# Kernel optimization log

Measured on AMD Instinct MI355X. Metric: run time of the kernel, lower is better.

## Reference

```python
import jax, jax.numpy as jnp
import numpy as np
import math

LOG_2PI = math.log(2.0 * math.pi)

def mv_gaussian_log_prob(value, mu, sig_diags, event_shape):
    # sig_diags acts as per-dim std (matches torch source: diff**2 / sig**2)
    diff = value - mu
    M = jnp.sum((diff / sig_diags) ** 2, axis=-1)
    half_log_det = jnp.sum(jnp.log(sig_diags), axis=-1)
    return -0.5 * (event_shape * LOG_2PI + M) - half_log_det

def setup_inputs() -> dict:
    key = jax.random.key(0)
    ks = jax.random.split(key, 18)
    N, Yd, Xd, K, S = 8192, 512, 64, 16, 10
    d = {}
    d['Y'] = jax.random.normal(ks[0], (N, Yd), jnp.float32)
    d['We_mu'] = jax.random.normal(ks[1], (Yd, Xd), jnp.float32) * 0.05
    d['be_mu'] = jnp.zeros((Xd,), jnp.float32)
    d['We_sig'] = jax.random.normal(ks[2], (Yd, Xd), jnp.float32) * 0.05
    d['be_sig'] = jnp.zeros((Xd,), jnp.float32)
    d['Wd_mu'] = jax.random.normal(ks[3], (Xd, Yd), jnp.float32) * 0.05
    d['bd_mu'] = jnp.zeros((Yd,), jnp.float32)
    d['Wd_sig'] = jax.random.normal(ks[4], (Xd, Yd), jnp.float32) * 0.05
    d['bd_sig'] = jnp.zeros((Yd,), jnp.float32)
    d['phi_mus'] = jax.random.normal(ks[5], (K, Xd), jnp.float32)
    d['phi_sigs'] = jax.random.uniform(ks[6], (K, Xd), jnp.float32, 0.5, 1.5)
    d['phi_logits'] = jax.random.normal(ks[7], (K,), jnp.float32)
    d['theta_mus'] = jax.random.normal(ks[8], (K, Xd), jnp.float32)
    d['theta_sigs'] = jax.random.uniform(ks[9], (K, Xd), jnp.float32, 0.5, 1.5)
    d['theta_logits'] = jax.random.normal(ks[10], (K,), jnp.float32)
    d['u_noise'] = jax.random.uniform(ks[11], (N, S, K), jnp.float32, 1e-6, 1.0 - 1e-6)
    d['eps_noise'] = jax.random.normal(ks[12], (N * S, Xd), jnp.float32)
    d['temperature'] = jnp.ones((1,), jnp.float32)
    return d

def reference(Y, We_mu, be_mu, We_sig, be_sig, Wd_mu, bd_mu, Wd_sig, bd_sig,
              phi_mus, phi_sigs, phi_logits, theta_mus, theta_sigs, theta_logits,
              u_noise, eps_noise, temperature):
    N, Yd = Y.shape
    K, Xd = phi_mus.shape
    S = u_noise.shape[1]
    # encoder: diagonal Gaussian q(x|y)
    enc_mu = Y @ We_mu + be_mu                                   # [N,Xd]
    enc_sig = jax.nn.softplus(Y @ We_sig + be_sig) + 1e-3        # [N,Xd]
    # cluster responsibilities (vectorized over k)
    log_pi = jax.nn.log_softmax(phi_logits)                      # [K]
    std_k = enc_sig[:, None, :] + phi_sigs[None, :, :]           # [N,K,Xd]
    z_logits = log_pi[None, :] + mv_gaussian_log_prob(
        enc_mu[:, None, :], phi_mus[None, :, :], std_k, Xd)      # [N,K]
    z_log_probs = jax.nn.log_softmax(z_logits, axis=-1)
    # per-cluster posterior (diagonal precision-weighted combination)
    inv_enc = 1.0 / enc_sig                                      # [N,Xd]
    inv_gmm = 1.0 / phi_sigs                                     # [K,Xd]
    Sig_t = 1.0 / (inv_enc[:, None, :] + inv_gmm[None, :, :])    # [N,K,Xd]
    mu_t = Sig_t * ((inv_enc * enc_mu)[:, None, :] + (inv_gmm * phi_mus)[None, :, :])
    # relaxed one-hot (gumbel-softmax) samples, probs = exp(z_log_probs)
    g = -jnp.log(-jnp.log(u_noise))                              # [N,S,K]
    z = jax.nn.softmax((z_log_probs[:, None, :] + g) / temperature[0], axis=-1)
    mu_s = jnp.einsum('bsk,bkd->bsd', z, mu_t).reshape(N * S, Xd)
    Sig_s = jnp.einsum('bsk,bkd->bsd', z, Sig_t).reshape(N * S, Xd)
    th_mu = jnp.einsum('bsk,kd->bsd', z, theta_mus).reshape(N * S, Xd)
    th_sig = jnp.einsum('bsk,kd->bsd', z, theta_sigs).reshape(N * S, Xd)
    ph_mu = jnp.einsum('bsk,kd->bsd', z, phi_mus).reshape(N * S, Xd)
    ph_sig = jnp.einsum('bsk,kd->bsd', z, phi_sigs).reshape(N * S, Xd)
    # reparameterized latent samples (diag cov -> std = sqrt)
    x_samp = mu_s + jnp.sqrt(Sig_s) * eps_noise                  # [N*S,Xd]
    # decoder
    mu_y = x_samp @ Wd_mu + bd_mu
    sig_y = jax.nn.softplus(x_samp @ Wd_sig + bd_sig) + 1e-3
    Yr = jnp.broadcast_to(Y[:, None, :], (N, S, Yd)).reshape(N * S, Yd)
    enc_mu_r = jnp.broadcast_to(enc_mu[:, None, :], (N, S, Xd)).reshape(N * S, Xd)
    enc_sig_r = jnp.broadcast_to(enc_sig[:, None, :], (N, S, Xd)).reshape(N * S, Xd)
    zf = z.reshape(N * S, K)
    loss1 = mv_gaussian_log_prob(Yr, mu_y, sig_y, Yd)
    loss2 = -mv_gaussian_log_prob(x_samp, enc_mu_r, enc_sig_r, Xd)
    loss3 = (mv_gaussian_log_prob(x_samp, th_mu, th_sig, Xd)
             + jnp.sum(jax.nn.log_softmax(theta_logits) * zf, axis=1))
    loss4 = -(mv_gaussian_log_prob(x_samp, ph_mu, ph_sig, Xd)
              + jnp.sum((z_log_probs[:, None, :] * z).reshape(N * S, K), axis=1))
    loss5 = jnp.sum(jnp.log(jnp.sum(jnp.exp(z_log_probs), axis=1)))
    return -(jnp.sum(loss1 + loss2 + loss3 + loss4) / S + loss5)
```

## Files before the change

kernel.cpp:

```cpp
#include <hip/hip_runtime.h>
#include <math.h>

#define YD 512
#define XD 64
#define KK 16

typedef __attribute__((ext_vector_type(8))) short short8;
typedef __attribute__((ext_vector_type(4))) float f32x4;

__device__ __forceinline__ float wave_sum(float v) {
#pragma unroll
    for (int off = 32; off > 0; off >>= 1) v += __shfl_xor(v, off, 64);
    return v;
}

__device__ __forceinline__ float fast_rcp(float x) {
    return __builtin_amdgcn_rcpf(x);
}

__device__ __forceinline__ float bcast(float v, int l) {
    return __uint_as_float((unsigned int)__builtin_amdgcn_readlane((int)__float_as_uint(v), l));
}

__device__ __forceinline__ float softplusf(float x) {
    return fmaxf(x, 0.0f) + __logf(1.0f + __expf(-fabsf(x)));
}

__device__ __forceinline__ unsigned short f32_to_bf16(float f) {
    union { float f; unsigned int u; } v; v.f = f;
    unsigned int r = v.u + 0x7fffu + ((v.u >> 16) & 1u);
    return (unsigned short)(r >> 16);
}

__device__ __forceinline__ unsigned int pack2_bf16(float a, float b) {
    unsigned int ua = __float_as_uint(a), ub = __float_as_uint(b);
    ua = (ua + 0x7fffu + ((ua >> 16) & 1u)) >> 16;
    ub = (ub + 0x7fffu + ((ub >> 16) & 1u)) & 0xffff0000u;
    return ua | ub;
}

__global__ __launch_bounds__(256) void prep_kernel(
    const float* __restrict__ Wd_mu, const float* __restrict__ Wd_sig,
    const float* __restrict__ We_mu, const float* __restrict__ We_sig,
    const float* __restrict__ phi_mus, const float* __restrict__ phi_sigs,
    const float* __restrict__ theta_mus, const float* __restrict__ theta_sigs,
    const float* __restrict__ theta_logits,
    unsigned short* __restrict__ wmu_s, unsigned short* __restrict__ wsg_s,
    unsigned short* __restrict__ wenc,
    float4* __restrict__ tab4, float* __restrict__ lsetp)
{
    int idx = blockIdx.x * 256 + threadIdx.x;
    if (idx < 65536) {
        int mat = idx >> 15;
        int e = idx & 32767;
        int j = e & 7;
        int n = (e >> 3) & 15;
        int q = (e >> 7) & 7;
        int tg = e >> 10;
        int k = q * 8 + j;
        int col = tg * 16 + n;
        const float* W = mat ? Wd_sig : Wd_mu;
        unsigned short* o = mat ? wsg_s : wmu_s;
        o[e] = f32_to_bf16(W[k * YD + col]);
    } else if (idx < 131072) {
        int ii = idx - 65536;
        int mat = ii >> 15;
        int e = ii & 32767;
        int j = e & 7;
        int n = (e >> 3) & 15;
        int q = (e >> 7) & 3;
        int ct = (e >> 9) & 3;
        int kt = e >> 11;
        int k = kt * 32 + q * 8 + j;
        int col = ct * 16 + n;
        const float* W = mat ? We_sig : We_mu;
        wenc[mat * 32768 + e] = f32_to_bf16(W[k * XD + col]);
    } else if (idx < 131072 + 1024) {
        int e = idx - 131072;
        float4 t;
        t.x = phi_mus[e];
        t.y = phi_sigs[e];
        t.z = theta_mus[e];
        t.w = theta_sigs[e];
        tab4[e] = t;
    } else if (idx == 131072 + 1024) {
        float mt = theta_logits[0];
        for (int k = 1; k < KK; ++k) mt = fmaxf(mt, theta_logits[k]);
        float st = 0.f;
        for (int k = 0; k < KK; ++k) st += __expf(theta_logits[k] - mt);
        lsetp[0] = mt + __logf(st);
    }
}

__global__ __launch_bounds__(256) void encoder_mfma(
    const float* __restrict__ Y,
    const unsigned short* __restrict__ wenc,
    const float* __restrict__ be_mu, const float* __restrict__ be_sig,
    float* __restrict__ enc_mu, float* __restrict__ enc_sig)
{
    const int t = threadIdx.x;
    const int w = t >> 6, lane = t & 63, l16 = lane & 15, quad = lane >> 4;
    const int mat = blockIdx.x & 1;
    const int rt = blockIdx.x >> 1;
    const int row = rt * 32 + (w >> 1) * 16 + l16;
    const int ct0 = (w & 1) * 2;
    const unsigned short* Ws = wenc + mat * 32768;
    const float4* Yrow = (const float4*)(Y + (size_t)row * YD);

    f32x4 acc0 = (f32x4){0.f, 0.f, 0.f, 0.f};
    f32x4 acc1 = (f32x4){0.f, 0.f, 0.f, 0.f};

#pragma unroll
    for (int kt = 0; kt < 16; ++kt) {
        float4 y0 = Yrow[kt * 8 + quad * 2];
        float4 y1 = Yrow[kt * 8 + quad * 2 + 1];
        union { short8 s; unsigned int u[4]; } a;
        a.u[0] = pack2_bf16(y0.x, y0.y);
        a.u[1] = pack2_bf16(y0.z, y0.w);
        a.u[2] = pack2_bf16(y1.x, y1.y);
        a.u[3] = pack2_bf16(y1.z, y1.w);
        short8 b0 = *(const short8*)(Ws + (((kt * 4 + ct0) * 4 + quad) * 16 + l16) * 8);
        short8 b1 = *(const short8*)(Ws + (((kt * 4 + ct0 + 1) * 4 + quad) * 16 + l16) * 8);
        acc0 = __builtin_amdgcn_mfma_f32_16x16x32_bf16(a.s, b0, acc0, 0, 0, 0);
        acc1 = __builtin_amdgcn_mfma_f32_16x16x32_bf16(a.s, b1, acc1, 0, 0, 0);
    }

    const float* bias = mat ? be_sig : be_mu;
    float* outp = mat ? enc_sig : enc_mu;
    const int base_row = rt * 32 + (w >> 1) * 16 + quad * 4;
#pragma unroll
    for (int h = 0; h < 2; ++h) {
        int col = (ct0 + h) * 16 + l16;
        float bv = bias[col];
        f32x4 acc = h ? acc1 : acc0;
#pragma unroll
        for (int r = 0; r < 4; ++r) {
            float v = acc[r] + bv;
            if (mat) v = softplusf(v) + 1e-3f;
            outp[(size_t)(base_row + r) * XD + col] = v;
        }
    }
}

__global__ __launch_bounds__(256) void resp_kernel(
    const float* __restrict__ enc_mu_g, const float* __restrict__ enc_sig_g,
    const float* __restrict__ phi_mus, const float* __restrict__ phi_sigs,
    const float* __restrict__ phi_logits,
    float* __restrict__ zlp, double* __restrict__ slotsL5)
{
    __shared__ float red[4];
    const int wv = threadIdx.x >> 6;
    const int n = blockIdx.x * 4 + wv;
    const int lane = threadIdx.x & 63;
    const int kk = lane & 15;
    const int g = lane >> 4;

    const float4* em4 = (const float4*)(enc_mu_g + (size_t)n * XD + g * 16);
    const float4* es4 = (const float4*)(enc_sig_g + (size_t)n * XD + g * 16);
    const float4* pm4 = (const float4*)(phi_mus + kk * XD + g * 16);
    const float4* ps4 = (const float4*)(phi_sigs + kk * XD + g * 16);

    float part = 0.f;
#pragma unroll
    for (int q = 0; q < 4; ++q) {
        float4 em = em4[q], es = es4[q], pm = pm4[q], ps = ps4[q];
        {
            float sd = es.x + ps.x; float df = (em.x - pm.x) * fast_rcp(sd);
            part += fmaf(-0.5f * df, df, -__logf(sd));
        }
        {
            float sd = es.y + ps.y; float df = (em.y - pm.y) * fast_rcp(sd);
            part += fmaf(-0.5f * df, df, -__logf(sd));
        }
        {
            float sd = es.z + ps.z; float df = (em.z - pm.z) * fast_rcp(sd);
            part += fmaf(-0.5f * df, df, -__logf(sd));
        }
        {
            float sd = es.w + ps.w; float df = (em.w - pm.w) * fast_rcp(sd);
            part += fmaf(-0.5f * df, df, -__logf(sd));
        }
    }
    part += __shfl_xor(part, 16, 64);
    part += __shfl_xor(part, 32, 64);
    float zl = part + phi_logits[kk];

    float m = zl;
#pragma unroll
    for (int off = 1; off <= 8; off <<= 1) m = fmaxf(m, __shfl_xor(m, off, 64));
    float e = __expf(zl - m);
    float s = e;
#pragma unroll
    for (int off = 1; off <= 8; off <<= 1) s += __shfl_xor(s, off, 64);
    zl -= m + __logf(s);

    float m3 = zl;
#pragma unroll
    for (int off = 1; off <= 8; off <<= 1) m3 = fmaxf(m3, __shfl_xor(m3, off, 64));
    float e3 = __expf(zl - m3);
    float s3 = e3;
#pragma unroll
    for (int off = 1; off <= 8; off <<= 1) s3 += __shfl_xor(s3, off, 64);
    float l5 = m3 + __logf(s3);

    if (lane < KK) zlp[(size_t)n * KK + lane] = zl;

    if (lane == 0) red[wv] = l5;
    __syncthreads();
    if (threadIdx.x == 0) {
        float tt = red[0] + red[1] + red[2] + red[3];
        atomicAdd(slotsL5 + (blockIdx.x & 63), (double)tt);
    }
}

__global__ __launch_bounds__(256, 6) void sample_kernel(
    const float* __restrict__ enc_mu_g, const float* __restrict__ enc_sig_g,
    const float* __restrict__ zlp, const float4* __restrict__ tab4,
    const float* __restrict__ theta_logits, const float* __restrict__ lsetp,
    const float* __restrict__ u_noise, const float* __restrict__ eps_noise,
    const float* __restrict__ temperature,
    unsigned short* __restrict__ x_bf16, double* __restrict__ slots234,
    unsigned int magicS)
{
    __shared__ float red[4];
    const int wv = threadIdx.x >> 6;
    const int wid = blockIdx.x * 4 + wv;
    const int d = threadIdx.x & 63;
    const int n = (int)(((unsigned long long)(unsigned int)wid * magicS) >> 35);

    const int kd = d & 15;
    const float invT = fast_rcp(temperature[0]);
    float zlk = zlp[(size_t)n * KK + kd];
    float u   = u_noise[(size_t)wid * KK + kd];
    float tlk = theta_logits[kd];
    float lgk = (zlk - __logf(-__logf(u))) * invT;
    float mg = lgk;
    mg = fmaxf(mg, __shfl_xor(mg, 1, 64));
    mg = fmaxf(mg, __shfl_xor(mg, 2, 64));
    mg = fmaxf(mg, __shfl_xor(mg, 4, 64));
    mg = fmaxf(mg, __shfl_xor(mg, 8, 64));
    float ek = __expf(lgk - mg);
    float zs = ek;
    float pz = ek * zlk;
    float pt = ek * tlk;
#pragma unroll
    for (int off = 1; off <= 8; off <<= 1) {
        zs += __shfl_xor(zs, off, 64);
        pz += __shfl_xor(pz, off, 64);
        pt += __shfl_xor(pt, off, 64);
    }
    const float rn   = fast_rcp(bcast(zs, 0));
    const float dzS  = bcast(pz, 0) * rn;
    const float dthS = bcast(pt, 0) * rn;

    const float em = enc_mu_g[(size_t)n * XD + d];
    const float es = enc_sig_g[(size_t)n * XD + d];
    const float inv_es = fast_rcp(es);
    const float log_es = __logf(es);
    const float em_ie = inv_es * em;

    float ms = 0.f, Ss = 0.f, tmu = 0.f, tsig = 0.f, pmu = 0.f, psig = 0.f;
#pragma unroll
    for (int k = 0; k < KK; ++k) {
        float e_k = bcast(ek, k);
        float4 tb = tab4[k * XD + d];
        float ig = fast_rcp(tb.y);
        float Sg = fast_rcp(inv_es + ig);
        float mu = Sg * fmaf(ig, tb.x, em_ie);
        ms   = fmaf(e_k, mu, ms);
        Ss   = fmaf(e_k, Sg, Ss);
        tmu  = fmaf(e_k, tb.z, tmu);
        tsig = fmaf(e_k, tb.w, tsig);
        pmu  = fmaf(e_k, tb.x, pmu);
        psig = fmaf(e_k, tb.y, psig);
    }
    ms *= rn; Ss *= rn; tmu *= rn; tsig *= rn; pmu *= rn; psig *= rn;

    float ep = eps_noise[(size_t)wid * XD + d];
    float x = fmaf(__builtin_amdgcn_sqrtf(Ss), ep, ms);
    x_bf16[(size_t)wid * XD + d] = f32_to_bf16(x);

    float de  = (x - em) * inv_es;
    float dt2 = (x - tmu) * fast_rcp(tsig);
    float dp  = (x - pmu) * fast_rcp(psig);
    float r = 0.5f * (de * de - dt2 * dt2 + dp * dp)
            + log_es - __logf(tsig) + __logf(psig);
    r = wave_sum(r);

    const float C234 = 0.5f * XD * 1.8378770664093453f;
    float acc = r + C234 + (dthS - lsetp[0]) - dzS;

    if (d == 0) red[wv] = acc;
    __syncthreads();
    if (threadIdx.x == 0) {
        float t = red[0] + red[1] + red[2] + red[3];
        atomicAdd(slots234 + (blockIdx.x & 63), (double)t);
    }
}

__global__ __launch_bounds__(256) void decoder_mfma(
    const unsigned short* __restrict__ xb,
    const unsigned short* __restrict__ wmu_s,
    const unsigned short* __restrict__ wsg_s,
    const float* __restrict__ bd_mu, const float* __restrict__ bd_sig,
    const float* __restrict__ Y, double* __restrict__ slots1,
    unsigned int magicS)
{
    __shared__ float red[4];
    const int t = threadIdx.x;
    const int w = t >> 6;
    const int lane = t & 63;
    const int l16 = lane & 15;
    const int quad = lane >> 4;
    const int mb = blockIdx.x >> 3;
    const int nb = blockIdx.x & 7;

    const int mrow = mb * 64 + w * 16 + l16;
    const short8 a0 = *(const short8*)(xb + (size_t)mrow * XD + quad * 8);
    const short8 a1 = *(const short8*)(xb + (size_t)mrow * XD + 32 + quad * 8);

    f32x4 accmu[4], accsg[4];
#pragma unroll
    for (int tt = 0; tt < 4; ++tt) {
        accmu[tt] = (f32x4){0.f, 0.f, 0.f, 0.f};
        accsg[tt] = (f32x4){0.f, 0.f, 0.f, 0.f};
    }

#pragma unroll
    for (int tt = 0; tt < 4; ++tt) {
        int tg = nb * 4 + tt;
        int boff = ((tg * 8 + quad) * 16 + l16) * 8;
        short8 b0 = *(const short8*)(wmu_s + boff);
        short8 b1 = *(const short8*)(wmu_s + boff + 512);
        short8 c0 = *(const short8*)(wsg_s + boff);
        short8 c1 = *(const short8*)(wsg_s + boff + 512);
        accmu[tt] = __builtin_amdgcn_mfma_f32_16x16x32_bf16(a0, b0, accmu[tt], 0, 0, 0);
        accmu[tt] = __builtin_amdgcn_mfma_f32_16x16x32_bf16(a1, b1, accmu[tt], 0, 0, 0);
        accsg[tt] = __builtin_amdgcn_mfma_f32_16x16x32_bf16(a0, c0, accsg[tt], 0, 0, 0);
        accsg[tt] = __builtin_amdgcn_mfma_f32_16x16x32_bf16(a1, c1, accsg[tt], 0, 0, 0);
    }

    float part = 0.f;
    const int m_base = mb * 64 + w * 16 + quad * 4;
#pragma unroll
    for (int tt = 0; tt < 4; ++tt) {
        int col = (nb * 4 + tt) * 16 + l16;
        float bmv = bd_mu[col], bsv = bd_sig[col];
#pragma unroll
        for (int r = 0; r < 4; ++r) {
            int row = m_base + r;
            unsigned int ny = (unsigned int)(((unsigned long long)(unsigned int)row * magicS) >> 35);
            float Yv = Y[(size_t)ny * YD + col];
            float sig = softplusf(accsg[tt][r] + bsv) + 1e-3f;
            float diff = (Yv - (accmu[tt][r] + bmv)) * fast_rcp(sig);
            part = fmaf(-0.5f * diff, diff, part) - __logf(sig);
        }
    }
    part = wave_sum(part);
    if (lane == 0) red[w] = part;
    __syncthreads();
    if (t == 0) {
        atomicAdd(slots1 + (blockIdx.x & 63),
                  (double)(red[0] + red[1] + red[2] + red[3]));
    }
}

__global__ void finalize_kernel(const double* __restrict__ slots,
                                float* __restrict__ out, int NS, int S)
{
    double l234 = 0.0, l5 = 0.0, l1 = 0.0;
    for (int i = 0; i < 64; ++i) {
        l234 += slots[i];
        l5   += slots[64 + i];
        l1   += slots[128 + i];
    }
    l1 += (double)NS * (-0.5 * (double)YD * 1.8378770664093453);
    out[0] = (float)(-((l1 + l234) / (double)S + l5));
}

extern "C" void kernel_launch(void* const* d_in, const int* in_sizes, int n_in,
                              void* d_out, int out_size, void* d_ws, size_t ws_size,
                              hipStream_t stream) {
    const float* Y            = (const float*)d_in[0];
    const float* We_mu        = (const float*)d_in[1];
    const float* be_mu        = (const float*)d_in[2];
    const float* We_sig       = (const float*)d_in[3];
    const float* be_sig       = (const float*)d_in[4];
    const float* Wd_mu        = (const float*)d_in[5];
    const float* bd_mu        = (const float*)d_in[6];
    const float* Wd_sig       = (const float*)d_in[7];
    const float* bd_sig       = (const float*)d_in[8];
    const float* phi_mus      = (const float*)d_in[9];
    const float* phi_sigs     = (const float*)d_in[10];
    const float* phi_logits   = (const float*)d_in[11];
    const float* theta_mus    = (const float*)d_in[12];
    const float* theta_sigs   = (const float*)d_in[13];
    const float* theta_logits = (const float*)d_in[14];
    const float* u_noise      = (const float*)d_in[15];
    const float* eps_noise    = (const float*)d_in[16];
    const float* temperature  = (const float*)d_in[17];

    const int N = in_sizes[0] / YD;
    const int S = in_sizes[15] / (N * KK);
    const int NS = N * S;
    const unsigned int magicS =
        (unsigned int)((((unsigned long long)1 << 35) + S - 1) / (unsigned long long)S);

    char* base = (char*)d_ws;
    double* slots = (double*)base;
    float* enc_mu  = (float*)(base + 2048);
    float* enc_sig = enc_mu + (size_t)N * XD;
    float* zlp     = enc_sig + (size_t)N * XD;
    float4* tab4   = (float4*)(zlp + (size_t)N * KK);
    float* lsetp   = (float*)(tab4 + 1024);
    unsigned short* xb    = (unsigned short*)(lsetp + 16);
    unsigned short* wmu_s = xb + (size_t)NS * XD;
    unsigned short* wsg_s = wmu_s + 32768;
    unsigned short* wenc  = wsg_s + 32768;

    hipMemsetAsync(slots, 0, 2048, stream);

    prep_kernel<<<517, 256, 0, stream>>>(Wd_mu, Wd_sig, We_mu, We_sig,
                                         phi_mus, phi_sigs, theta_mus,
                                         theta_sigs, theta_logits,
                                         wmu_s, wsg_s, wenc, tab4, lsetp);
    encoder_mfma<<<(N / 32) * 2, 256, 0, stream>>>(Y, wenc, be_mu, be_sig,
                                                   enc_mu, enc_sig);
    resp_kernel<<<N / 4, 256, 0, stream>>>(enc_mu, enc_sig, phi_mus, phi_sigs,
                                           phi_logits, zlp, slots + 64);
    sample_kernel<<<NS / 4, 256, 0, stream>>>(enc_mu, enc_sig, zlp, tab4,
                                              theta_logits, lsetp,
                                              u_noise, eps_noise, temperature,
                                              xb, slots, magicS);
    decoder_mfma<<<(NS / 64) * (YD / 64), 256, 0, stream>>>(
        xb, wmu_s, wsg_s, bd_mu, bd_sig, Y, slots + 128, magicS);
    finalize_kernel<<<1, 1, 0, stream>>>(slots, (float*)d_out, NS, S);
}
```

Before: 240.3 us.

## Process all samples per data row in sample kernel, reusing per-cluster posterior terms

The sample kernel now assigns one wave per data row and loops over all S samples, so the per-cluster posterior mean/variance, theta/phi tables and encoder stats are computed and loaded once per row instead of once per sample. Gumbel-softmax weights for up to four samples are computed in parallel across 16-lane groups. Register use rises (six 16-entry arrays), so the occupancy hint drops from 6 to 3. The encoder is split into one 16-column tile per wave with twice as many blocks, and biases are folded into the MFMA accumulator init in both the encoder and decoder.

```diff
diff --git a/kernel.cpp b/kernel.cpp
--- a/kernel.cpp
+++ b/kernel.cpp
@@ -4,6 +4,7 @@
 #define YD 512
 #define XD 64
 #define KK 16
+#define SS 10
 
 typedef __attribute__((ext_vector_type(8))) short short8;
 typedef __attribute__((ext_vector_type(4))) float f32x4;
@@ -102,13 +103,16 @@
     const int w = t >> 6, lane = t & 63, l16 = lane & 15, quad = lane >> 4;
     const int mat = blockIdx.x & 1;
     const int rt = blockIdx.x >> 1;
-    const int row = rt * 32 + (w >> 1) * 16 + l16;
-    const int ct0 = (w & 1) * 2;
+    const int row = rt * 16 + l16;
+    const int ct = w;
     const unsigned short* Ws = wenc + mat * 32768;
     const float4* Yrow = (const float4*)(Y + (size_t)row * YD);
 
-    f32x4 acc0 = (f32x4){0.f, 0.f, 0.f, 0.f};
-    f32x4 acc1 = (f32x4){0.f, 0.f, 0.f, 0.f};
+    const float* bias = mat ? be_sig : be_mu;
+    float* outp = mat ? enc_sig : enc_mu;
+    const int col = ct * 16 + l16;
+    const float bv = bias[col];
+    f32x4 acc = (f32x4){bv, bv, bv, bv};
 
 #pragma unroll
     for (int kt = 0; kt < 16; ++kt) {
@@ -119,26 +123,16 @@
         a.u[1] = pack2_bf16(y0.z, y0.w);
         a.u[2] = pack2_bf16(y1.x, y1.y);
         a.u[3] = pack2_bf16(y1.z, y1.w);
-        short8 b0 = *(const short8*)(Ws + (((kt * 4 + ct0) * 4 + quad) * 16 + l16) * 8);
-        short8 b1 = *(const short8*)(Ws + (((kt * 4 + ct0 + 1) * 4 + quad) * 16 + l16) * 8);
-        acc0 = __builtin_amdgcn_mfma_f32_16x16x32_bf16(a.s, b0, acc0, 0, 0, 0);
-        acc1 = __builtin_amdgcn_mfma_f32_16x16x32_bf16(a.s, b1, acc1, 0, 0, 0);
-    }
-
-    const float* bias = mat ? be_sig : be_mu;
-    float* outp = mat ? enc_sig : enc_mu;
-    const int base_row = rt * 32 + (w >> 1) * 16 + quad * 4;
-#pragma unroll
-    for (int h = 0; h < 2; ++h) {
-        int col = (ct0 + h) * 16 + l16;
-        float bv = bias[col];
-        f32x4 acc = h ? acc1 : acc0;
-#pragma unroll
-        for (int r = 0; r < 4; ++r) {
-            float v = acc[r] + bv;
-            if (mat) v = softplusf(v) + 1e-3f;
-            outp[(size_t)(base_row + r) * XD + col] = v;
-        }
+        short8 b = *(const short8*)(Ws + (((kt * 4 + ct) * 4 + quad) * 16 + l16) * 8);
+        acc = __builtin_amdgcn_mfma_f32_16x16x32_bf16(a.s, b, acc, 0, 0, 0);
+    }
+
+    const int base_row = rt * 16 + quad * 4;
+#pragma unroll
+    for (int r = 0; r < 4; ++r) {
+        float v = acc[r];
+        if (mat) v = softplusf(v) + 1e-3f;
+        outp[(size_t)(base_row + r) * XD + col] = v;
     }
 }
 
@@ -213,45 +207,24 @@
     }
 }
 
-__global__ __launch_bounds__(256, 6) void sample_kernel(
+__global__ __launch_bounds__(256, 3) void sample_kernel(
     const float* __restrict__ enc_mu_g, const float* __restrict__ enc_sig_g,
     const float* __restrict__ zlp, const float4* __restrict__ tab4,
     const float* __restrict__ theta_logits, const float* __restrict__ lsetp,
     const float* __restrict__ u_noise, const float* __restrict__ eps_noise,
     const float* __restrict__ temperature,
-    unsigned short* __restrict__ x_bf16, double* __restrict__ slots234,
-    unsigned int magicS)
+    unsigned short* __restrict__ x_bf16, double* __restrict__ slots234)
 {
     __shared__ float red[4];
     const int wv = threadIdx.x >> 6;
-    const int wid = blockIdx.x * 4 + wv;
+    const int n = blockIdx.x * 4 + wv;
     const int d = threadIdx.x & 63;
-    const int n = (int)(((unsigned long long)(unsigned int)wid * magicS) >> 35);
-
     const int kd = d & 15;
+
     const float invT = fast_rcp(temperature[0]);
-    float zlk = zlp[(size_t)n * KK + kd];
-    float u   = u_noise[(size_t)wid * KK + kd];
-    float tlk = theta_logits[kd];
-    float lgk = (zlk - __logf(-__logf(u))) * invT;
-    float mg = lgk;
-    mg = fmaxf(mg, __shfl_xor(mg, 1, 64));
-    mg = fmaxf(mg, __shfl_xor(mg, 2, 64));
-    mg = fmaxf(mg, __shfl_xor(mg, 4, 64));
-    mg = fmaxf(mg, __shfl_xor(mg, 8, 64));
-    float ek = __expf(lgk - mg);
-    float zs = ek;
-    float pz = ek * zlk;
-    float pt = ek * tlk;
-#pragma unroll
-    for (int off = 1; off <= 8; off <<= 1) {
-        zs += __shfl_xor(zs, off, 64);
-        pz += __shfl_xor(pz, off, 64);
-        pt += __shfl_xor(pt, off, 64);
-    }
-    const float rn   = fast_rcp(bcast(zs, 0));
-    const float dzS  = bcast(pz, 0) * rn;
-    const float dthS = bcast(pt, 0) * rn;
+    const float zl_l = zlp[(size_t)n * KK + kd];
+    const float tl_l = theta_logits[kd];
+    const float lset = lsetp[0];
 
     const float em = enc_mu_g[(size_t)n * XD + d];
     const float es = enc_sig_g[(size_t)n * XD + d];
@@ -259,38 +232,81 @@
     const float log_es = __logf(es);
     const float em_ie = inv_es * em;
 
-    float ms = 0.f, Ss = 0.f, tmu = 0.f, tsig = 0.f, pmu = 0.f, psig = 0.f;
+    float mu[KK], Sg[KK], tm[KK], ts[KK], pm[KK], ps[KK];
 #pragma unroll
     for (int k = 0; k < KK; ++k) {
-        float e_k = bcast(ek, k);
         float4 tb = tab4[k * XD + d];
+        pm[k] = tb.x; ps[k] = tb.y; tm[k] = tb.z; ts[k] = tb.w;
         float ig = fast_rcp(tb.y);
-        float Sg = fast_rcp(inv_es + ig);
-        float mu = Sg * fmaf(ig, tb.x, em_ie);
-        ms   = fmaf(e_k, mu, ms);
-        Ss   = fmaf(e_k, Sg, Ss);
-        tmu  = fmaf(e_k, tb.z, tmu);
-        tsig = fmaf(e_k, tb.w, tsig);
-        pmu  = fmaf(e_k, tb.x, pmu);
-        psig = fmaf(e_k, tb.y, psig);
-    }
-    ms *= rn; Ss *= rn; tmu *= rn; tsig *= rn; pmu *= rn; psig *= rn;
-
-    float ep = eps_noise[(size_t)wid * XD + d];
-    float x = fmaf(__builtin_amdgcn_sqrtf(Ss), ep, ms);
-    x_bf16[(size_t)wid * XD + d] = f32_to_bf16(x);
-
-    float de  = (x - em) * inv_es;
-    float dt2 = (x - tmu) * fast_rcp(tsig);
-    float dp  = (x - pmu) * fast_rcp(psig);
-    float r = 0.5f * (de * de - dt2 * dt2 + dp * dp)
-            + log_es - __logf(tsig) + __logf(psig);
-    r = wave_sum(r);
+        Sg[k] = fast_rcp(inv_es + ig);
+        mu[k] = Sg[k] * fmaf(ig, tb.x, em_ie);
+    }
+
+    float eP[3], dzP[3], dthP[3];
+#pragma unroll
+    for (int p = 0; p < 3; ++p) {
+        int sp = p * 4 + (d >> 4);
+        int spc = sp < SS ? sp : 0;
+        float u = u_noise[((size_t)n * SS + spc) * KK + kd];
+        float lg = (zl_l - __logf(-__logf(u))) * invT;
+        float mg = lg;
+        mg = fmaxf(mg, __shfl_xor(mg, 1, 64));
+        mg = fmaxf(mg, __shfl_xor(mg, 2, 64));
+        mg = fmaxf(mg, __shfl_xor(mg, 4, 64));
+        mg = fmaxf(mg, __shfl_xor(mg, 8, 64));
+        float e = __expf(lg - mg);
+        float zs = e;
+        zs += __shfl_xor(zs, 1, 64);
+        zs += __shfl_xor(zs, 2, 64);
+        zs += __shfl_xor(zs, 4, 64);
+        zs += __shfl_xor(zs, 8, 64);
+        e *= fast_rcp(zs);
+        float pz = e * zl_l, pt = e * tl_l;
+#pragma unroll
+        for (int off = 1; off <= 8; off <<= 1) {
+            pz += __shfl_xor(pz, off, 64);
+            pt += __shfl_xor(pt, off, 64);
+        }
+        eP[p] = e; dzP[p] = pz; dthP[p] = pt;
+    }
+
+    float r_acc = 0.f, sc_acc = 0.f;
+    const float* erow = eps_noise + (size_t)n * SS * XD + d;
+    unsigned short* xrow = x_bf16 + (size_t)n * SS * XD + d;
+
+#pragma unroll
+    for (int s = 0; s < SS; ++s) {
+        const int p = s >> 2, L = (s & 3) * 16;
+        float ms = 0.f, Ssum = 0.f, tmu = 0.f, tsig = 0.f, pmu = 0.f, psig = 0.f;
+#pragma unroll
+        for (int k = 0; k < KK; ++k) {
+            float ek = bcast(eP[p], L + k);
+            ms   = fmaf(ek, mu[k], ms);
+            Ssum = fmaf(ek, Sg[k], Ssum);
+            tmu  = fmaf(ek, tm[k], tmu);
+            tsig = fmaf(ek, ts[k], tsig);
+            pmu  = fmaf(ek, pm[k], pmu);
+            psig = fmaf(ek, ps[k], psig);
+        }
+        float ep = erow[s * XD];
+        float x = fmaf(__builtin_amdgcn_sqrtf(Ssum), ep, ms);
+        xrow[s * XD] = f32_to_bf16(x);
+
+        float de  = (x - em) * inv_es;
+        float rts = fast_rcp(tsig);
+        float dt2 = (x - tmu) * rts;
+        float dp  = (x - pmu) * fast_rcp(psig);
+        r_acc += 0.5f * (de * de - dt2 * dt2 + dp * dp) + __logf(psig * rts);
+        sc_acc += bcast(dthP[p], L) - bcast(dzP[p], L);
+    }
+
+    r_acc = fmaf((float)SS, log_es, r_acc);
+    r_acc = wave_sum(r_acc);
 
     const float C234 = 0.5f * XD * 1.8378770664093453f;
-    float acc = r + C234 + (dthS - lsetp[0]) - dzS;
-
-    if (d == 0) red[wv] = acc;
+    float total = r_acc + sc_acc + (float)SS * (C234 - lset);
+
+    if (d == 0) red[wv] = total;
     __syncthreads();
     if (threadIdx.x == 0) {
         float t = red[0] + red[1] + red[2] + red[3];
@@ -322,8 +338,10 @@
     f32x4 accmu[4], accsg[4];
 #pragma unroll
     for (int tt = 0; tt < 4; ++tt) {
-        accmu[tt] = (f32x4){0.f, 0.f, 0.f, 0.f};
-        accsg[tt] = (f32x4){0.f, 0.f, 0.f, 0.f};
+        int col = (nb * 4 + tt) * 16 + l16;
+        float bm = bd_mu[col], bs = bd_sig[col];
+        accmu[tt] = (f32x4){bm, bm, bm, bm};
+        accsg[tt] = (f32x4){bs, bs, bs, bs};
     }
 
 #pragma unroll
@@ -343,16 +361,15 @@
     float part = 0.f;
     const int m_base = mb * 64 + w * 16 + quad * 4;
 #pragma unroll
-    for (int tt = 0; tt < 4; ++tt) {
-        int col = (nb * 4 + tt) * 16 + l16;
-        float bmv = bd_mu[col], bsv = bd_sig[col];
-#pragma unroll
-        for (int r = 0; r < 4; ++r) {
-            int row = m_base + r;
-            unsigned int ny = (unsigned int)(((unsigned long long)(unsigned int)row * magicS) >> 35);
-            float Yv = Y[(size_t)ny * YD + col];
-            float sig = softplusf(accsg[tt][r] + bsv) + 1e-3f;
-            float diff = (Yv - (accmu[tt][r] + bmv)) * fast_rcp(sig);
+    for (int r = 0; r < 4; ++r) {
+        int row = m_base + r;
+        unsigned int ny = (unsigned int)(((unsigned long long)(unsigned int)row * magicS) >> 35);
+        const float* Yr = Y + (size_t)ny * YD + l16;
+#pragma unroll
+        for (int tt = 0; tt < 4; ++tt) {
+            float Yv = Yr[(nb * 4 + tt) * 16];
+            float sig = softplusf(accsg[tt][r]) + 1e-3f;
+            float diff = (Yv - accmu[tt][r]) * fast_rcp(sig);
             part = fmaf(-0.5f * diff, diff, part) - __logf(sig);
         }
     }
@@ -424,14 +441,14 @@
                                          phi_mus, phi_sigs, theta_mus,
                                          theta_sigs, theta_logits,
                                          wmu_s, wsg_s, wenc, tab4, lsetp);
-    encoder_mfma<<<(N / 32) * 2, 256, 0, stream>>>(Y, wenc, be_mu, be_sig,
+    encoder_mfma<<<(N / 16) * 2, 256, 0, stream>>>(Y, wenc, be_mu, be_sig,
                                                    enc_mu, enc_sig);
     resp_kernel<<<N / 4, 256, 0, stream>>>(enc_mu, enc_sig, phi_mus, phi_sigs,
                                            phi_logits, zlp, slots + 64);
-    sample_kernel<<<NS / 4, 256, 0, stream>>>(enc_mu, enc_sig, zlp, tab4,
-                                              theta_logits, lsetp,
-                                              u_noise, eps_noise, temperature,
-                                              xb, slots, magicS);
+    sample_kernel<<<N / 4, 256, 0, stream>>>(enc_mu, enc_sig, zlp, tab4,
+                                             theta_logits, lsetp,
+                                             u_noise, eps_noise, temperature,
+                                             xb, slots);
     decoder_mfma<<<(NS / 64) * (YD / 64), 256, 0, stream>>>(
         xb, wmu_s, wsg_s, bd_mu, bd_sig, Y, slots + 128, magicS);
     finalize_kernel<<<1, 1, 0, stream>>>(slots, (float*)d_out, NS, S);
```

New measurement: 220.3 us. 1.09x faster.
